# Kernel optimization log

Measured on AMD Instinct MI355X. Metric: run time of the kernel, lower is better.

## Reference

```python
import jax, jax.numpy as jnp
import numpy as np

B = 131072      # batch
D_IN = 256      # cfg.input_dim
H = 512         # hidden width
D_OUT = 128     # cfg.output_dim
ALPHA = 0.2     # cfg.alpha
EPS = 1e-6      # cfg.eps
K_MAX = 1000    # cfg.k_max


def _init_linear(k, shape, fan_in):
    lim = 1.0 / np.sqrt(fan_in)
    return jax.random.uniform(k, shape, jnp.float32, -lim, lim)


def setup_inputs() -> dict:
    key = jax.random.key(0)
    ks = jax.random.split(key, 7)
    return {
        "x": jax.random.normal(ks[0], (B, D_IN), jnp.float32),
        "W1": _init_linear(ks[1], (D_IN, H), D_IN),
        "b1": _init_linear(ks[2], (H,), D_IN),
        "W2": _init_linear(ks[3], (H, H), H),
        "b2": _init_linear(ks[4], (H,), H),
        "W3": _init_linear(ks[5], (H, D_OUT), H),
        "b3": _init_linear(ks[6], (D_OUT,), H),
    }


def _mlp(x, W1, b1, W2, b2, W3, b3):
    # MLP with tanh activations (cfg.act_F='tanh'), final layer linear
    h = jnp.tanh(x @ W1 + b1)
    h = jnp.tanh(h @ W2 + b2)
    return h @ W3 + b3  # (B, D_OUT)


def _fixed_point(F_x):
    # y_{k+1} = y_k + alpha * tanh(F_x - y_k); break when max_b ||y_{k+1}-y_k||_2 < eps
    y0 = jnp.zeros_like(F_x)

    def cond(state):
        y, k, done = state
        return (k < K_MAX) & (~done)

    def body(state):
        y, k, done = state
        y_next = y + ALPHA * jnp.tanh(F_x - y)
        step = jnp.sqrt(jnp.sum(jnp.square(y_next - y), axis=1))  # (B,)
        done = jnp.max(step) < EPS
        return (y_next, k + 1, done)

    y, _, _ = jax.lax.while_loop(cond, body, (y0, jnp.int32(0), jnp.bool_(False)))
    return y


def reference(x, W1, b1, W2, b2, W3, b3):
    F_x = _mlp(x, W1, b1, W2, b2, W3, b3)
    return _fixed_point(F_x)
```

## Files before the change

### kernel.cpp

```cpp
#include <hip/hip_runtime.h>

typedef short s16x8 __attribute__((ext_vector_type(8)));
typedef unsigned short u16x8 __attribute__((ext_vector_type(8)));
typedef float f32x16 __attribute__((ext_vector_type(16)));

__device__ __forceinline__ unsigned short f2bf(float f) {
  unsigned u = __float_as_uint(f);
  u += 0x7fffu + ((u >> 16) & 1u);
  return (unsigned short)(u >> 16);
}

__device__ __forceinline__ float tanh_fast(float x) {
  float xc = fminf(15.f, fmaxf(-15.f, x));
  float t = __builtin_amdgcn_exp2f(xc * 2.8853900817779268f);
  return (t - 1.f) * __builtin_amdgcn_rcpf(t + 1.f);
}

__global__ __launch_bounds__(256)
void prep_pack(const float* __restrict__ W1, const float* __restrict__ W2,
               const float* __restrict__ W3, unsigned short* __restrict__ ws) {
  __shared__ unsigned short t[64][65];
  const int b = blockIdx.x;
  const float* W; unsigned short* base; int KK, N, tk, tn;
  if (b < 32)      { W = W1; base = ws;          KK = 16; N = 512; tk = b >> 3;       tn = b & 7; }
  else if (b < 96) { int g = b - 32; W = W2; base = ws + 131072; KK = 32; N = 512; tk = g >> 3; tn = g & 7; }
  else             { int g = b - 96; W = W3; base = ws + 393216; KK = 32; N = 128; tk = g >> 1; tn = g & 1; }

  const int tid = threadIdx.x;
  #pragma unroll
  for (int p = 0; p < 16; ++p) {
    int kl = p * 4 + (tid >> 6);
    int nl = tid & 63;
    t[kl][nl] = f2bf(W[(size_t)(tk * 64 + kl) * N + tn * 64 + nl]);
  }
  __syncthreads();

  const int lane = tid & 63, ln31 = lane & 31, khalf = lane >> 5;
  #pragma unroll
  for (int pass = 0; pass < 2; ++pass) {
    int pair = pass * 4 + (tid >> 6);
    int tn_l = pair & 1, kk_l = pair >> 1;
    int tile = tn * 2 + tn_l, kk = tk * 4 + kk_l;
    u16x8 v;
    #pragma unroll
    for (int j = 0; j < 8; ++j)
      v[j] = t[kk_l * 16 + khalf * 8 + j][tn_l * 32 + ln31];
    *(u16x8*)(base + ((size_t)(tile * KK + kk) * 64 + lane) * 8) = v;
  }
}

#define ABASE(row) ((row) * 512 + ((row) & 7) * 8)

#define BAR() asm volatile("s_waitcnt lgkmcnt(0)\n\ts_barrier" ::: "memory")

__global__ __launch_bounds__(512, 4)
void mlp_limit_kernel(const float* __restrict__ x,
                      const float* __restrict__ b1, const float* __restrict__ b2,
                      const float* __restrict__ b3,
                      const unsigned short* __restrict__ w1p,
                      const unsigned short* __restrict__ w2p,
                      const unsigned short* __restrict__ w3p,
                      float* __restrict__ out) {
  __shared__ __align__(16) unsigned short lds[64 * 512];
  const int tid   = threadIdx.x;
  const int w     = __builtin_amdgcn_readfirstlane(tid >> 6);
  const int lane  = tid & 63;
  const int ln31  = lane & 31;
  const int khalf = lane >> 5;
  const int m0    = blockIdx.x * 64;

  const s16x8* bpL1_0 = (const s16x8*)w1p + (size_t)((w * 2 + 0) * 16) * 64 + lane;
  const s16x8* bpL1_1 = (const s16x8*)w1p + (size_t)((w * 2 + 1) * 16) * 64 + lane;
  s16x8 bb0[2], bb1[2];
  bb0[0] = bpL1_0[0];  bb1[0] = bpL1_1[0];
  bb0[1] = bpL1_0[64]; bb1[1] = bpL1_1[64];

  #pragma unroll
  for (int c = tid; c < 2048; c += 512) {
    int row = c >> 5, ch = c & 31;
    const float4* src = (const float4*)(x + (size_t)(m0 + row) * 256 + ch * 8);
    float4 f0 = src[0], f1 = src[1];
    u16x8 v;
    v[0] = f2bf(f0.x); v[1] = f2bf(f0.y); v[2] = f2bf(f0.z); v[3] = f2bf(f0.w);
    v[4] = f2bf(f1.x); v[5] = f2bf(f1.y); v[6] = f2bf(f1.z); v[7] = f2bf(f1.w);
    *(u16x8*)&lds[row * 512 + ((ch ^ (row & 7)) * 8)] = v;
  }
  BAR();

  const int abase0 = ABASE(ln31);
  const int abase1 = ABASE(ln31 + 32);
  const int ncb    = w * 64;
  const int kh32   = khalf * 32;
  const int khA    = khalf * 8;

  f32x16 acc[2][2];

  #pragma unroll
  for (int mt = 0; mt < 2; ++mt)
    #pragma unroll
    for (int nt = 0; nt < 2; ++nt)
      #pragma unroll
      for (int r = 0; r < 16; ++r) acc[mt][nt][r] = 0.f;
  {
    s16x8 a0[2], a1[2];
    a0[0] = *(const s16x8*)&lds[abase0 ^ khA];
    a1[0] = *(const s16x8*)&lds[abase1 ^ khA];
    #pragma unroll
    for (int kk = 0; kk < 16; ++kk) {
      const int s = kk & 1, d = s ^ 1;
      if (kk + 1 < 16) {
        a0[d] = *(const s16x8*)&lds[abase0 ^ ((kk + 1) * 16 + khA)];
        a1[d] = *(const s16x8*)&lds[abase1 ^ ((kk + 1) * 16 + khA)];
      }
      acc[0][0] = __builtin_amdgcn_mfma_f32_32x32x16_bf16(a0[s], bb0[s], acc[0][0], 0, 0, 0);
      acc[0][1] = __builtin_amdgcn_mfma_f32_32x32x16_bf16(a0[s], bb1[s], acc[0][1], 0, 0, 0);
      acc[1][0] = __builtin_amdgcn_mfma_f32_32x32x16_bf16(a1[s], bb0[s], acc[1][0], 0, 0, 0);
      acc[1][1] = __builtin_amdgcn_mfma_f32_32x32x16_bf16(a1[s], bb1[s], acc[1][1], 0, 0, 0);
      if (kk + 2 < 16) {
        bb0[s] = bpL1_0[(kk + 2) * 64];
        bb1[s] = bpL1_1[(kk + 2) * 64];
      }
    }
  }

  const s16x8* bpL2_0 = (const s16x8*)w2p + (size_t)((w * 2 + 0) * 32) * 64 + lane;
  const s16x8* bpL2_1 = (const s16x8*)w2p + (size_t)((w * 2 + 1) * 32) * 64 + lane;
  bb0[0] = bpL2_0[0];  bb1[0] = bpL2_1[0];
  bb0[1] = bpL2_0[64]; bb1[1] = bpL2_1[64];
  float bias1[2] = { b1[ncb + ln31], b1[ncb + 32 + ln31] };

  BAR();

  #pragma unroll
  for (int nt = 0; nt < 2; ++nt) {
    int hc = ncb + nt * 32 + ln31;
    int wi = hc & 7;
    int e  = (((hc >> 3) * 8) ^ kh32) + wi + khalf * 2048;
    #pragma unroll
    for (int mt = 0; mt < 2; ++mt)
      #pragma unroll
      for (int r = 0; r < 16; ++r) {
        int C = (mt * 32 + (r & 3) + 8 * (r >> 2)) * 512;
        lds[C + (e ^ ((r & 3) * 8))] = f2bf(tanh_fast(acc[mt][nt][r] + bias1[nt]));
      }
  }
  BAR();

  #pragma unroll
  for (int mt = 0; mt < 2; ++mt)
    #pragma unroll
    for (int nt = 0; nt < 2; ++nt)
      #pragma unroll
      for (int r = 0; r < 16; ++r) acc[mt][nt][r] = 0.f;
  {
    s16x8 a0[2], a1[2];
    a0[0] = *(const s16x8*)&lds[abase0 ^ khA];
    a1[0] = *(const s16x8*)&lds[abase1 ^ khA];
    #pragma unroll
    for (int kk = 0; kk < 32; ++kk) {
      const int s = kk & 1, d = s ^ 1;
      if (kk + 1 < 32) {
        a0[d] = *(const s16x8*)&lds[abase0 ^ ((kk + 1) * 16 + khA)];
        a1[d] = *(const s16x8*)&lds[abase1 ^ ((kk + 1) * 16 + khA)];
      }
      acc[0][0] = __builtin_amdgcn_mfma_f32_32x32x16_bf16(a0[s], bb0[s], acc[0][0], 0, 0, 0);
      acc[0][1] = __builtin_amdgcn_mfma_f32_32x32x16_bf16(a0[s], bb1[s], acc[0][1], 0, 0, 0);
      acc[1][0] = __builtin_amdgcn_mfma_f32_32x32x16_bf16(a1[s], bb0[s], acc[1][0], 0, 0, 0);
      acc[1][1] = __builtin_amdgcn_mfma_f32_32x32x16_bf16(a1[s], bb1[s], acc[1][1], 0, 0, 0);
      if (kk + 2 < 32) {
        bb0[s] = bpL2_0[(kk + 2) * 64];
        bb1[s] = bpL2_1[(kk + 2) * 64];
      }
    }
  }

  const int t3 = w & 3;
  const int mh = (w >> 2) * 32;
  const s16x8* bpL3 = (const s16x8*)w3p + (size_t)(t3 * 32) * 64 + lane;
  s16x8 b3r[3];
  b3r[0] = bpL3[0]; b3r[1] = bpL3[64]; b3r[2] = bpL3[128];
  float bias2[2] = { b2[ncb + ln31], b2[ncb + 32 + ln31] };
  float bz = b3[t3 * 32 + ln31];

  BAR();

  #pragma unroll
  for (int nt = 0; nt < 2; ++nt) {
    int hc = ncb + nt * 32 + ln31;
    int wi = hc & 7;
    int e  = (((hc >> 3) * 8) ^ kh32) + wi + khalf * 2048;
    #pragma unroll
    for (int mt = 0; mt < 2; ++mt)
      #pragma unroll
      for (int r = 0; r < 16; ++r) {
        int C = (mt * 32 + (r & 3) + 8 * (r >> 2)) * 512;
        lds[C + (e ^ ((r & 3) * 8))] = f2bf(tanh_fast(acc[mt][nt][r] + bias2[nt]));
      }
  }
  BAR();

  {
    const int ab = ABASE(mh + ln31);
    f32x16 acc3;
    #pragma unroll
    for (int r = 0; r < 16; ++r) acc3[r] = 0.f;
    s16x8 a3[3];
    a3[0] = *(const s16x8*)&lds[ab ^ (0 * 16 + khA)];
    a3[1] = *(const s16x8*)&lds[ab ^ (1 * 16 + khA)];
    a3[2] = *(const s16x8*)&lds[ab ^ (2 * 16 + khA)];
    #pragma unroll
    for (int kk = 0; kk < 32; ++kk) {
      const int s = kk % 3;
      acc3 = __builtin_amdgcn_mfma_f32_32x32x16_bf16(a3[s], b3r[s], acc3, 0, 0, 0);
      if (kk + 3 < 32) {
        a3[s]  = *(const s16x8*)&lds[ab ^ ((kk + 3) * 16 + khA)];
        b3r[s] = bpL3[(kk + 3) * 64];
      }
    }
    #pragma unroll
    for (int r = 0; r < 16; ++r) {
      int m = m0 + mh + (r & 3) + 8 * (r >> 2) + 4 * khalf;
      out[(size_t)m * 128 + t3 * 32 + ln31] = acc3[r] + bz;
    }
  }
}

extern "C" void kernel_launch(void* const* d_in, const int* in_sizes, int n_in,
                              void* d_out, int out_size, void* d_ws, size_t ws_size,
                              hipStream_t stream) {
  const float* x  = (const float*)d_in[0];
  const float* W1 = (const float*)d_in[1];
  const float* b1 = (const float*)d_in[2];
  const float* W2 = (const float*)d_in[3];
  const float* b2 = (const float*)d_in[4];
  const float* W3 = (const float*)d_in[5];
  const float* b3 = (const float*)d_in[6];
  float* out = (float*)d_out;
  unsigned short* ws = (unsigned short*)d_ws;

  hipLaunchKernelGGL(prep_pack, dim3(112), dim3(256), 0, stream, W1, W2, W3, ws);
  hipLaunchKernelGGL(mlp_limit_kernel, dim3(2048), dim3(512), 0, stream,
                     x, b1, b2, b3, ws, ws + 131072, ws + 393216, out);
}
```

Measured before the change: 342.9 us.

## Double the block to 1024 threads over 128 rows and fold biases into accumulator init

The fused MLP kernel now runs 16 waves per block over 128 batch rows instead of 8 waves over 64, with LDS doubled to 128 KB. Waves split into two row halves that share the same weight-column slices. Biases now seed the MFMA accumulators rather than being added in the epilogue, and the tanh lower clamp is dropped. The larger block halves the grid and aims for more reuse and less per-block overhead, but the launch bound of 1024 threads with a hint of 4 blocks may cap the register budget hard and force spills. LDS use also now limits the kernel to one block per CU.

```diff
diff --git a/kernel.cpp b/kernel.cpp
--- a/kernel.cpp
+++ b/kernel.cpp
@@ -11,7 +11,7 @@
 }
 
 __device__ __forceinline__ float tanh_fast(float x) {
-  float xc = fminf(15.f, fmaxf(-15.f, x));
+  float xc = fminf(15.f, x);
   float t = __builtin_amdgcn_exp2f(xc * 2.8853900817779268f);
   return (t - 1.f) * __builtin_amdgcn_rcpf(t + 1.f);
 }
@@ -53,7 +53,7 @@
 
 #define BAR() asm volatile("s_waitcnt lgkmcnt(0)\n\ts_barrier" ::: "memory")
 
-__global__ __launch_bounds__(512, 4)
+__global__ __launch_bounds__(1024, 4)
 void mlp_limit_kernel(const float* __restrict__ x,
                       const float* __restrict__ b1, const float* __restrict__ b2,
                       const float* __restrict__ b3,
@@ -61,22 +61,27 @@
                       const unsigned short* __restrict__ w2p,
                       const unsigned short* __restrict__ w3p,
                       float* __restrict__ out) {
-  __shared__ __align__(16) unsigned short lds[64 * 512];
+  __shared__ __align__(16) unsigned short lds[128 * 512];
   const int tid   = threadIdx.x;
   const int w     = __builtin_amdgcn_readfirstlane(tid >> 6);
   const int lane  = tid & 63;
   const int ln31  = lane & 31;
   const int khalf = lane >> 5;
-  const int m0    = blockIdx.x * 64;
-
-  const s16x8* bpL1_0 = (const s16x8*)w1p + (size_t)((w * 2 + 0) * 16) * 64 + lane;
-  const s16x8* bpL1_1 = (const s16x8*)w1p + (size_t)((w * 2 + 1) * 16) * 64 + lane;
+  const int m0    = blockIdx.x * 128;
+
+  const int nw    = w & 7;
+  const int mhalf = w >> 3;
+  const int ncb   = nw * 64;
+
+  const s16x8* bpL1_0 = (const s16x8*)w1p + (size_t)((nw * 2 + 0) * 16) * 64 + lane;
+  const s16x8* bpL1_1 = (const s16x8*)w1p + (size_t)((nw * 2 + 1) * 16) * 64 + lane;
   s16x8 bb0[2], bb1[2];
   bb0[0] = bpL1_0[0];  bb1[0] = bpL1_1[0];
   bb0[1] = bpL1_0[64]; bb1[1] = bpL1_1[64];
-
-  #pragma unroll
-  for (int c = tid; c < 2048; c += 512) {
+  float bias1v[2] = { b1[ncb + ln31], b1[ncb + 32 + ln31] };
+
+  #pragma unroll
+  for (int c = tid; c < 4096; c += 1024) {
     int row = c >> 5, ch = c & 31;
     const float4* src = (const float4*)(x + (size_t)(m0 + row) * 256 + ch * 8);
     float4 f0 = src[0], f1 = src[1];
@@ -87,11 +92,11 @@
   }
   BAR();
 
-  const int abase0 = ABASE(ln31);
-  const int abase1 = ABASE(ln31 + 32);
-  const int ncb    = w * 64;
+  const int abase0 = ABASE(mhalf * 64 + ln31);
+  const int abase1 = ABASE(mhalf * 64 + 32 + ln31);
   const int kh32   = khalf * 32;
   const int khA    = khalf * 8;
+  const int mrow0  = mhalf * 64;
 
   f32x16 acc[2][2];
 
@@ -100,7 +105,7 @@
     #pragma unroll
     for (int nt = 0; nt < 2; ++nt)
       #pragma unroll
-      for (int r = 0; r < 16; ++r) acc[mt][nt][r] = 0.f;
+      for (int r = 0; r < 16; ++r) acc[mt][nt][r] = bias1v[nt];
   {
     s16x8 a0[2], a1[2];
     a0[0] = *(const s16x8*)&lds[abase0 ^ khA];
@@ -123,11 +128,11 @@
     }
   }
 
-  const s16x8* bpL2_0 = (const s16x8*)w2p + (size_t)((w * 2 + 0) * 32) * 64 + lane;
-  const s16x8* bpL2_1 = (const s16x8*)w2p + (size_t)((w * 2 + 1) * 32) * 64 + lane;
+  const s16x8* bpL2_0 = (const s16x8*)w2p + (size_t)((nw * 2 + 0) * 32) * 64 + lane;
+  const s16x8* bpL2_1 = (const s16x8*)w2p + (size_t)((nw * 2 + 1) * 32) * 64 + lane;
   bb0[0] = bpL2_0[0];  bb1[0] = bpL2_1[0];
   bb0[1] = bpL2_0[64]; bb1[1] = bpL2_1[64];
-  float bias1[2] = { b1[ncb + ln31], b1[ncb + 32 + ln31] };
+  float bias2v[2] = { b2[ncb + ln31], b2[ncb + 32 + ln31] };
 
   BAR();
 
@@ -140,8 +145,8 @@
     for (int mt = 0; mt < 2; ++mt)
       #pragma unroll
       for (int r = 0; r < 16; ++r) {
-        int C = (mt * 32 + (r & 3) + 8 * (r >> 2)) * 512;
-        lds[C + (e ^ ((r & 3) * 8))] = f2bf(tanh_fast(acc[mt][nt][r] + bias1[nt]));
+        int C = (mrow0 + mt * 32 + (r & 3) + 8 * (r >> 2)) * 512;
+        lds[C + (e ^ ((r & 3) * 8))] = f2bf(tanh_fast(acc[mt][nt][r]));
       }
   }
   BAR();
@@ -151,7 +156,7 @@
     #pragma unroll
     for (int nt = 0; nt < 2; ++nt)
       #pragma unroll
-      for (int r = 0; r < 16; ++r) acc[mt][nt][r] = 0.f;
+      for (int r = 0; r < 16; ++r) acc[mt][nt][r] = bias2v[nt];
   {
     s16x8 a0[2], a1[2];
     a0[0] = *(const s16x8*)&lds[abase0 ^ khA];
@@ -179,7 +184,6 @@
   const s16x8* bpL3 = (const s16x8*)w3p + (size_t)(t3 * 32) * 64 + lane;
   s16x8 b3r[3];
   b3r[0] = bpL3[0]; b3r[1] = bpL3[64]; b3r[2] = bpL3[128];
-  float bias2[2] = { b2[ncb + ln31], b2[ncb + 32 + ln31] };
   float bz = b3[t3 * 32 + ln31];
 
   BAR();
@@ -193,8 +197,8 @@
     for (int mt = 0; mt < 2; ++mt)
       #pragma unroll
       for (int r = 0; r < 16; ++r) {
-        int C = (mt * 32 + (r & 3) + 8 * (r >> 2)) * 512;
-        lds[C + (e ^ ((r & 3) * 8))] = f2bf(tanh_fast(acc[mt][nt][r] + bias2[nt]));
+        int C = (mrow0 + mt * 32 + (r & 3) + 8 * (r >> 2)) * 512;
+        lds[C + (e ^ ((r & 3) * 8))] = f2bf(tanh_fast(acc[mt][nt][r]));
       }
   }
   BAR();
@@ -203,7 +207,7 @@
     const int ab = ABASE(mh + ln31);
     f32x16 acc3;
     #pragma unroll
-    for (int r = 0; r < 16; ++r) acc3[r] = 0.f;
+    for (int r = 0; r < 16; ++r) acc3[r] = bz;
     s16x8 a3[3];
     a3[0] = *(const s16x8*)&lds[ab ^ (0 * 16 + khA)];
     a3[1] = *(const s16x8*)&lds[ab ^ (1 * 16 + khA)];
@@ -220,7 +224,7 @@
     #pragma unroll
     for (int r = 0; r < 16; ++r) {
       int m = m0 + mh + (r & 3) + 8 * (r >> 2) + 4 * khalf;
-      out[(size_t)m * 128 + t3 * 32 + ln31] = acc3[r] + bz;
+      out[(size_t)m * 128 + t3 * 32 + ln31] = acc3[r];
     }
   }
 }
@@ -239,6 +243,6 @@
   unsigned short* ws = (unsigned short*)d_ws;
 
   hipLaunchKernelGGL(prep_pack, dim3(112), dim3(256), 0, stream, W1, W2, W3, ws);
-  hipLaunchKernelGGL(mlp_limit_kernel, dim3(2048), dim3(512), 0, stream,
+  hipLaunchKernelGGL(mlp_limit_kernel, dim3(1024), dim3(1024), 0, stream,
                      x, b1, b2, b3, ws, ws + 131072, ws + 393216, out);
 }
```

After: 361.0 us. +5.3%, slower.

## Transpose MFMA operands so epilogue writes packed bf16 vectors to LDS

Applied to the files above, without the earlier changes.

Swaps the A/B operands of the layer-1 and layer-2 MFMAs so each lane holds consecutive hidden-column outputs. A new epilogue converts pairs with v_cvt_pk_bf16_f32, exchanges halves with v_permlane32_swap, and writes 16-byte vectors to swizzled LDS instead of scalar 2-byte stores. Input conversion also uses the packed bf16 instruction, the tanh lower clamp is dropped, and the layer-3 bias is folded into the accumulator init. This aims to cut LDS store count and epilogue ALU work, at the cost of relying on inline asm and changed accumulator layout semantics.

```diff
diff --git a/kernel.cpp b/kernel.cpp
--- a/kernel.cpp
+++ b/kernel.cpp
@@ -11,7 +11,7 @@
 }
 
 __device__ __forceinline__ float tanh_fast(float x) {
-  float xc = fminf(15.f, fmaxf(-15.f, x));
+  float xc = fminf(15.f, x);
   float t = __builtin_amdgcn_exp2f(xc * 2.8853900817779268f);
   return (t - 1.f) * __builtin_amdgcn_rcpf(t + 1.f);
 }
@@ -52,6 +52,42 @@
 #define ABASE(row) ((row) * 512 + ((row) & 7) * 8)
 
 #define BAR() asm volatile("s_waitcnt lgkmcnt(0)\n\ts_barrier" ::: "memory")
+
+__device__ __forceinline__ void ep_store(unsigned short* lds, const f32x16 acc[2][2],
+                                         const float* __restrict__ bptr,
+                                         int ncb, int ln31, int khalf) {
+  #pragma unroll
+  for (int ht = 0; ht < 2; ++ht) {
+    const int hcb = ncb + ht * 32;
+    float4 bs[4];
+    #pragma unroll
+    for (int g = 0; g < 4; ++g)
+      bs[g] = *(const float4*)&bptr[hcb + g * 8 + 4 * khalf];
+    #pragma unroll
+    for (int bt = 0; bt < 2; ++bt) {
+      const int row = bt * 32 + ln31;
+      const int rb = row * 512, swz = row & 7;
+      #pragma unroll
+      for (int kb = 0; kb < 2; ++kb) {
+        float v[8];
+        #pragma unroll
+        for (int j = 0; j < 8; ++j)
+          v[j] = tanh_fast(acc[ht][bt][kb * 8 + j] +
+                           ((const float*)&bs[kb * 2 + (j >> 2)])[j & 3]);
+        int w0, w1, w2, w3;
+        asm("v_cvt_pk_bf16_f32 %0, %1, %2" : "=v"(w0) : "v"(v[0]), "v"(v[1]));
+        asm("v_cvt_pk_bf16_f32 %0, %1, %2" : "=v"(w1) : "v"(v[2]), "v"(v[3]));
+        asm("v_cvt_pk_bf16_f32 %0, %1, %2" : "=v"(w2) : "v"(v[4]), "v"(v[5]));
+        asm("v_cvt_pk_bf16_f32 %0, %1, %2" : "=v"(w3) : "v"(v[6]), "v"(v[7]));
+        asm("v_permlane32_swap_b32 %0, %1" : "+v"(w0), "+v"(w2));
+        asm("v_permlane32_swap_b32 %0, %1" : "+v"(w1), "+v"(w3));
+        const int ch = (hcb >> 3) + 2 * kb + khalf;
+        int4 pk = { w0, w1, w2, w3 };
+        *(int4*)&lds[rb + ((ch ^ swz) * 8)] = pk;
+      }
+    }
+  }
+}
 
 __global__ __launch_bounds__(512, 4)
 void mlp_limit_kernel(const float* __restrict__ x,
@@ -80,27 +116,29 @@
     int row = c >> 5, ch = c & 31;
     const float4* src = (const float4*)(x + (size_t)(m0 + row) * 256 + ch * 8);
     float4 f0 = src[0], f1 = src[1];
-    u16x8 v;
-    v[0] = f2bf(f0.x); v[1] = f2bf(f0.y); v[2] = f2bf(f0.z); v[3] = f2bf(f0.w);
-    v[4] = f2bf(f1.x); v[5] = f2bf(f1.y); v[6] = f2bf(f1.z); v[7] = f2bf(f1.w);
-    *(u16x8*)&lds[row * 512 + ((ch ^ (row & 7)) * 8)] = v;
+    int q0, q1, q2, q3;
+    asm("v_cvt_pk_bf16_f32 %0, %1, %2" : "=v"(q0) : "v"(f0.x), "v"(f0.y));
+    asm("v_cvt_pk_bf16_f32 %0, %1, %2" : "=v"(q1) : "v"(f0.z), "v"(f0.w));
+    asm("v_cvt_pk_bf16_f32 %0, %1, %2" : "=v"(q2) : "v"(f1.x), "v"(f1.y));
+    asm("v_cvt_pk_bf16_f32 %0, %1, %2" : "=v"(q3) : "v"(f1.z), "v"(f1.w));
+    int4 pk = { q0, q1, q2, q3 };
+    *(int4*)&lds[row * 512 + ((ch ^ (row & 7)) * 8)] = pk;
   }
   BAR();
 
   const int abase0 = ABASE(ln31);
   const int abase1 = ABASE(ln31 + 32);
   const int ncb    = w * 64;
-  const int kh32   = khalf * 32;
   const int khA    = khalf * 8;
 
   f32x16 acc[2][2];
 
   #pragma unroll
-  for (int mt = 0; mt < 2; ++mt)
-    #pragma unroll
-    for (int nt = 0; nt < 2; ++nt)
+  for (int ht = 0; ht < 2; ++ht)
+    #pragma unroll
+    for (int bt = 0; bt < 2; ++bt)
       #pragma unroll
-      for (int r = 0; r < 16; ++r) acc[mt][nt][r] = 0.f;
+      for (int r = 0; r < 16; ++r) acc[ht][bt][r] = 0.f;
   {
     s16x8 a0[2], a1[2];
     a0[0] = *(const s16x8*)&lds[abase0 ^ khA];
@@ -112,10 +150,10 @@
         a0[d] = *(const s16x8*)&lds[abase0 ^ ((kk + 1) * 16 + khA)];
         a1[d] = *(const s16x8*)&lds[abase1 ^ ((kk + 1) * 16 + khA)];
       }
-      acc[0][0] = __builtin_amdgcn_mfma_f32_32x32x16_bf16(a0[s], bb0[s], acc[0][0], 0, 0, 0);
-      acc[0][1] = __builtin_amdgcn_mfma_f32_32x32x16_bf16(a0[s], bb1[s], acc[0][1], 0, 0, 0);
-      acc[1][0] = __builtin_amdgcn_mfma_f32_32x32x16_bf16(a1[s], bb0[s], acc[1][0], 0, 0, 0);
-      acc[1][1] = __builtin_amdgcn_mfma_f32_32x32x16_bf16(a1[s], bb1[s], acc[1][1], 0, 0, 0);
+      acc[0][0] = __builtin_amdgcn_mfma_f32_32x32x16_bf16(bb0[s], a0[s], acc[0][0], 0, 0, 0);
+      acc[0][1] = __builtin_amdgcn_mfma_f32_32x32x16_bf16(bb0[s], a1[s], acc[0][1], 0, 0, 0);
+      acc[1][0] = __builtin_amdgcn_mfma_f32_32x32x16_bf16(bb1[s], a0[s], acc[1][0], 0, 0, 0);
+      acc[1][1] = __builtin_amdgcn_mfma_f32_32x32x16_bf16(bb1[s], a1[s], acc[1][1], 0, 0, 0);
       if (kk + 2 < 16) {
         bb0[s] = bpL1_0[(kk + 2) * 64];
         bb1[s] = bpL1_1[(kk + 2) * 64];
@@ -127,31 +165,18 @@
   const s16x8* bpL2_1 = (const s16x8*)w2p + (size_t)((w * 2 + 1) * 32) * 64 + lane;
   bb0[0] = bpL2_0[0];  bb1[0] = bpL2_1[0];
   bb0[1] = bpL2_0[64]; bb1[1] = bpL2_1[64];
-  float bias1[2] = { b1[ncb + ln31], b1[ncb + 32 + ln31] };
-
-  BAR();
-
-  #pragma unroll
-  for (int nt = 0; nt < 2; ++nt) {
-    int hc = ncb + nt * 32 + ln31;
-    int wi = hc & 7;
-    int e  = (((hc >> 3) * 8) ^ kh32) + wi + khalf * 2048;
-    #pragma unroll
-    for (int mt = 0; mt < 2; ++mt)
+
+  BAR();
+
+  ep_store(lds, acc, b1, ncb, ln31, khalf);
+  BAR();
+
+  #pragma unroll
+  for (int ht = 0; ht < 2; ++ht)
+    #pragma unroll
+    for (int bt = 0; bt < 2; ++bt)
       #pragma unroll
-      for (int r = 0; r < 16; ++r) {
-        int C = (mt * 32 + (r & 3) + 8 * (r >> 2)) * 512;
-        lds[C + (e ^ ((r & 3) * 8))] = f2bf(tanh_fast(acc[mt][nt][r] + bias1[nt]));
-      }
-  }
-  BAR();
-
-  #pragma unroll
-  for (int mt = 0; mt < 2; ++mt)
-    #pragma unroll
-    for (int nt = 0; nt < 2; ++nt)
-      #pragma unroll
-      for (int r = 0; r < 16; ++r) acc[mt][nt][r] = 0.f;
+      for (int r = 0; r < 16; ++r) acc[ht][bt][r] = 0.f;
   {
     s16x8 a0[2], a1[2];
     a0[0] = *(const s16x8*)&lds[abase0 ^ khA];
@@ -163,10 +188,10 @@
         a0[d] = *(const s16x8*)&lds[abase0 ^ ((kk + 1) * 16 + khA)];
         a1[d] = *(const s16x8*)&lds[abase1 ^ ((kk + 1) * 16 + khA)];
       }
-      acc[0][0] = __builtin_amdgcn_mfma_f32_32x32x16_bf16(a0[s], bb0[s], acc[0][0], 0, 0, 0);
-      acc[0][1] = __builtin_amdgcn_mfma_f32_32x32x16_bf16(a0[s], bb1[s], acc[0][1], 0, 0, 0);
-      acc[1][0] = __builtin_amdgcn_mfma_f32_32x32x16_bf16(a1[s], bb0[s], acc[1][0], 0, 0, 0);
-      acc[1][1] = __builtin_amdgcn_mfma_f32_32x32x16_bf16(a1[s], bb1[s], acc[1][1], 0, 0, 0);
+      acc[0][0] = __builtin_amdgcn_mfma_f32_32x32x16_bf16(bb0[s], a0[s], acc[0][0], 0, 0, 0);
+      acc[0][1] = __builtin_amdgcn_mfma_f32_32x32x16_bf16(bb0[s], a1[s], acc[0][1], 0, 0, 0);
+      acc[1][0] = __builtin_amdgcn_mfma_f32_32x32x16_bf16(bb1[s], a0[s], acc[1][0], 0, 0, 0);
+      acc[1][1] = __builtin_amdgcn_mfma_f32_32x32x16_bf16(bb1[s], a1[s], acc[1][1], 0, 0, 0);
       if (kk + 2 < 32) {
         bb0[s] = bpL2_0[(kk + 2) * 64];
         bb1[s] = bpL2_1[(kk + 2) * 64];
@@ -179,31 +204,18 @@
   const s16x8* bpL3 = (const s16x8*)w3p + (size_t)(t3 * 32) * 64 + lane;
   s16x8 b3r[3];
   b3r[0] = bpL3[0]; b3r[1] = bpL3[64]; b3r[2] = bpL3[128];
-  float bias2[2] = { b2[ncb + ln31], b2[ncb + 32 + ln31] };
   float bz = b3[t3 * 32 + ln31];
 
   BAR();
 
-  #pragma unroll
-  for (int nt = 0; nt < 2; ++nt) {
-    int hc = ncb + nt * 32 + ln31;
-    int wi = hc & 7;
-    int e  = (((hc >> 3) * 8) ^ kh32) + wi + khalf * 2048;
-    #pragma unroll
-    for (int mt = 0; mt < 2; ++mt)
-      #pragma unroll
-      for (int r = 0; r < 16; ++r) {
-        int C = (mt * 32 + (r & 3) + 8 * (r >> 2)) * 512;
-        lds[C + (e ^ ((r & 3) * 8))] = f2bf(tanh_fast(acc[mt][nt][r] + bias2[nt]));
-      }
-  }
+  ep_store(lds, acc, b2, ncb, ln31, khalf);
   BAR();
 
   {
     const int ab = ABASE(mh + ln31);
     f32x16 acc3;
     #pragma unroll
-    for (int r = 0; r < 16; ++r) acc3[r] = 0.f;
+    for (int r = 0; r < 16; ++r) acc3[r] = bz;
     s16x8 a3[3];
     a3[0] = *(const s16x8*)&lds[ab ^ (0 * 16 + khA)];
     a3[1] = *(const s16x8*)&lds[ab ^ (1 * 16 + khA)];
@@ -220,7 +232,7 @@
     #pragma unroll
     for (int r = 0; r < 16; ++r) {
       int m = m0 + mh + (r & 3) + 8 * (r >> 2) + 4 * khalf;
-      out[(size_t)m * 128 + t3 * 32 + ln31] = acc3[r] + bz;
+      out[(size_t)m * 128 + t3 * 32 + ln31] = acc3[r];
     }
   }
 }
```

New measurement: 383.3 us. 11.8% more time.
